# Kernel optimization log

Hardware: AMD Instinct MI355X
Metric: run time of the kernel (lower is better)

The kernel has to match this reference:

```python
import jax, jax.numpy as jnp
import numpy as np

PAD = -2.0 ** 16 + 1.0  # tf code uses -2**16+1 as masked logit
ITERATIONS = 3


def squash(x):
    # x: [..., out_units]
    n = jnp.sum(jnp.square(x), axis=-1, keepdims=True)
    return (n / (1.0 + n) / jnp.sqrt(n + 1e-9)) * x


def setup_inputs() -> dict:
    key = jax.random.key(0)
    k1, k2, k3, k4 = jax.random.split(key, 4)
    B, L, DIN, DOUT, K = 4096, 200, 64, 64, 8
    return {
        "low_capsule": jax.random.normal(k1, (B, L, DIN), dtype=jnp.float32),
        "seq_len": jax.random.randint(k2, (B, 1), 1, L + 1, dtype=jnp.int32),
        "B_matrix": jax.random.normal(k3, (1, K, L), dtype=jnp.float32),
        "S_matrix": jax.random.normal(k4, (DIN, DOUT), dtype=jnp.float32),
    }


def reference(low_capsule, seq_len, B_matrix, S_matrix):
    # low_capsule: [B, L, Din]; seq_len: [B, 1]; B_matrix: [1, K, L]; S_matrix: [Din, Dout]
    L = B_matrix.shape[2]
    # tf.sequence_mask(tile(seq_len,[1,K]), L) -> [B, K, L]; K axis broadcasts.
    mask = jnp.arange(L)[None, None, :] < seq_len[:, :, None]  # [B, 1, L]
    # low_capsule_new is identical every iteration; compute once.
    low_new = jnp.einsum('bli,io->blo', low_capsule, S_matrix)  # [B, L, Dout]
    Bc = B_matrix  # routing logits, updated (stateful assign_add in tf)
    high = None
    for _ in range(ITERATIONS):
        logits = jnp.where(mask, Bc, PAD)  # [B, K, L]
        W = jax.nn.softmax(logits, axis=-1)
        high = squash(jnp.einsum('bkl,blo->bko', W, low_new))  # [B, K, Dout]
        # B_delta = sum_b high @ low_new^T, keepdims on batch
        Bc = Bc + jnp.einsum('bko,blo->kl', high, low_new)[None]  # [1, K, L]
    return high
```

## Files before the change

### kernel.cpp

```cpp
#include <hip/hip_runtime.h>
#include <math.h>


#define B_SZ  4096
#define L_SZ  200
#define DK    64
#define K_SZ  8
#define KL    1600

__device__ __forceinline__ float rl(float x, int i) {
    return __int_as_float(__builtin_amdgcn_readlane(__float_as_int(x), i));
}

template<int INIT, int WRITE_BC>
__global__ __launch_bounds__(256) void k_table(const float* __restrict__ Bm,
                                               const float* __restrict__ S,
                                               const float* __restrict__ p2,
                                               const float* __restrict__ BcIn,
                                               float* __restrict__ BcOut,
                                               float* __restrict__ St,
                                               float* __restrict__ Wt) {
    int t = threadIdx.x;
    int blk = blockIdx.x;
    if (INIT && blk == 200) {
        for (int j = t; j < DK * DK; j += 256) {
            int o = j >> 6, ii = j & 63;
            St[j] = S[ii * DK + o];
        }
        return;
    }
    __shared__ float Bv[KL];
    __shared__ float mArr[K_SZ], rArr[K_SZ];
    int s = blk + 1;

    for (int j = t; j < KL; j += 256) {
        float bn;
        if (INIT) {
            bn = Bm[j];
        } else {
            float acc = 0.f;
            #pragma unroll
            for (int y = 0; y < 16; ++y) acc += p2[y * KL + j];
            bn = BcIn[j] + acc;
            if (WRITE_BC && blk == 0) BcOut[j] = bn;
        }
        Bv[j] = bn;
    }
    __syncthreads();

    int k = t >> 5, g = t & 31;
    const float* bk = &Bv[k * L_SZ];
    float m = -3.4e38f;
    for (int l = g; l < s; l += 32) m = fmaxf(m, bk[l]);
    #pragma unroll
    for (int st = 16; st; st >>= 1) m = fmaxf(m, __shfl_xor(m, st, 32));
    float sum = 0.f;
    for (int l = g; l < s; l += 32) sum += __expf(bk[l] - m);
    #pragma unroll
    for (int st = 16; st; st >>= 1) sum += __shfl_xor(sum, st, 32);
    if (g == 0) { mArr[k] = m; rArr[k] = 1.0f / sum; }
    __syncthreads();

    float* dst = Wt + (long)(s - 1) * KL;
    for (int j = t; j < KL; j += 256) {
        int l = j >> 3, kk = j & 7;
        dst[j] = (l < s) ? __expf(Bv[kk * L_SZ + l] - mArr[kk]) * rArr[kk] : 0.f;
    }
}

template<int WRITE_OUT>
__global__ __launch_bounds__(256, 6) void k_route6(const float* __restrict__ lc_g,
                                                   const int* __restrict__ seq_len,
                                                   const float* __restrict__ Wt_g,
                                                   const float* __restrict__ S_g,
                                                   const float* __restrict__ St_g,
                                                   float* __restrict__ partial,
                                                   float* __restrict__ out) {
    __shared__ float Wl[KL];
    __shared__ float hp_part[4][K_SZ][DK];
    __shared__ float hp_s[K_SZ][DK];
    __shared__ float hs_s[K_SZ][DK];
    int t = threadIdx.x;
    int b = blockIdx.x;
    const float* __restrict__ lcb = lc_g + (long)b * (L_SZ * DK);
    const float4* __restrict__ lc4 = (const float4*)lcb;
    int sl = seq_len[b];

    {
        const float4* __restrict__ src =
            (const float4*)(Wt_g + (long)(sl - 1) * KL);
        float4* dst = (float4*)Wl;
        for (int j = t; j < KL / 4; j += 256) dst[j] = src[j];
    }
    __syncthreads();

    int grp = t >> 4;
    int w = t >> 6;
    float4 a[8];
    #pragma unroll
    for (int p = 0; p < 8; ++p) a[p] = make_float4(0.f, 0.f, 0.f, 0.f);

    #pragma unroll 4
    for (int j = 0; j < 12; ++j) {
        float4 v = lc4[t + 256 * j];
        int r = grp + 16 * j;
        float4 wa = *(const float4*)&Wl[r * 8];
        float4 wb = *(const float4*)&Wl[r * 8 + 4];
        float wk[8] = {wa.x, wa.y, wa.z, wa.w, wb.x, wb.y, wb.z, wb.w};
        #pragma unroll
        for (int p = 0; p < 8; ++p) {
            a[p].x = fmaf(wk[p], v.x, a[p].x);
            a[p].y = fmaf(wk[p], v.y, a[p].y);
            a[p].z = fmaf(wk[p], v.z, a[p].z);
            a[p].w = fmaf(wk[p], v.w, a[p].w);
        }
    }
    if (t < 128) {
        float4 v = lc4[t + 3072];
        int r = grp + 192;
        float4 wa = *(const float4*)&Wl[r * 8];
        float4 wb = *(const float4*)&Wl[r * 8 + 4];
        float wk[8] = {wa.x, wa.y, wa.z, wa.w, wb.x, wb.y, wb.z, wb.w};
        #pragma unroll
        for (int p = 0; p < 8; ++p) {
            a[p].x = fmaf(wk[p], v.x, a[p].x);
            a[p].y = fmaf(wk[p], v.y, a[p].y);
            a[p].z = fmaf(wk[p], v.z, a[p].z);
            a[p].w = fmaf(wk[p], v.w, a[p].w);
        }
    }

    #pragma unroll
    for (int p = 0; p < 8; ++p) {
        a[p].x += __shfl_xor(a[p].x, 16, 64);
        a[p].y += __shfl_xor(a[p].y, 16, 64);
        a[p].z += __shfl_xor(a[p].z, 16, 64);
        a[p].w += __shfl_xor(a[p].w, 16, 64);
        a[p].x += __shfl_xor(a[p].x, 32, 64);
        a[p].y += __shfl_xor(a[p].y, 32, 64);
        a[p].z += __shfl_xor(a[p].z, 32, 64);
        a[p].w += __shfl_xor(a[p].w, 32, 64);
    }
    if ((t & 63) < 16) {
        int c0 = (t & 15) * 4;
        #pragma unroll
        for (int p = 0; p < 8; ++p)
            *(float4*)&hp_part[w][p][c0] = a[p];
    }
    __syncthreads();

    {
        int kk = t >> 5, ii = (t & 31) * 2;
        float2 r2 = make_float2(0.f, 0.f);
        #pragma unroll
        for (int ww = 0; ww < 4; ++ww) {
            float2 p = *(const float2*)&hp_part[ww][kk][ii];
            r2.x += p.x; r2.y += p.y;
        }
        *(float2*)&hp_s[kk][ii] = r2;
    }
    __syncthreads();

    int k = t >> 5, g = t & 31;
    int lam = t & 63;
    float h0 = 0.f, h1 = 0.f;
    {
        const float* sp = S_g + 2 * g;
        #pragma unroll 8
        for (int i = 0; i < DK; ++i) {
            float pv = hp_s[k][i];
            float2 sv = *(const float2*)(sp + i * DK);
            h0 = fmaf(pv, sv.x, h0); h1 = fmaf(pv, sv.y, h1);
        }
        float nn = h0 * h0 + h1 * h1;
        #pragma unroll
        for (int st = 16; st; st >>= 1) nn += __shfl_xor(nn, st, 32);
        float sc = nn / ((1.0f + nn) * sqrtf(nn + 1e-9f));
        h0 *= sc; h1 *= sc;
    }
    if (WRITE_OUT) {
        float2* ob2 = (float2*)(out + (long)b * (K_SZ * DK) + k * DK);
        ob2[g] = make_float2(h0, h1);
        return;
    }
    *(float2*)&hp_s[k][2 * g] = make_float2(h0, h1);

    {
        float s0 = 0.f, s1 = 0.f;
        const float* stp = St_g + 2 * g;
        #pragma unroll 8
        for (int o = 0; o < DK; ++o) {
            float hv = hp_s[k][o];
            float2 sv = *(const float2*)(stp + o * DK);
            s0 = fmaf(hv, sv.x, s0); s1 = fmaf(hv, sv.y, s1);
        }
        *(float2*)&hs_s[k][2 * g] = make_float2(s0, s1);
    }
    __syncthreads();

    float hsr[K_SZ];
    #pragma unroll
    for (int kk = 0; kk < K_SZ; ++kk) hsr[kk] = hs_s[kk][lam];
    if (t < L_SZ) {
        const float4* row4 = (const float4*)(lcb + (long)t * DK);
        float aa[K_SZ] = {};
        #pragma unroll
        for (int i4 = 0; i4 < 16; ++i4) {
            float4 v = row4[i4];
            #pragma unroll
            for (int kk = 0; kk < K_SZ; ++kk) {
                aa[kk] = fmaf(rl(hsr[kk], 4 * i4 + 0), v.x,
                         fmaf(rl(hsr[kk], 4 * i4 + 1), v.y,
                         fmaf(rl(hsr[kk], 4 * i4 + 2), v.z,
                         fmaf(rl(hsr[kk], 4 * i4 + 3), v.w, aa[kk]))));
            }
        }
        float* pb = partial + (long)b * KL;
        #pragma unroll
        for (int kk = 0; kk < K_SZ; ++kk)
            pb[kk * L_SZ + t] = aa[kk];
    }
}

__global__ __launch_bounds__(256) void k_reduceA(const float* __restrict__ partial,
                                                 float* __restrict__ partial2) {
    __shared__ float red[256];
    int x = blockIdx.x % 50;
    int y = blockIdx.x / 50;
    int t = threadIdx.x;
    int i = x * 32 + (t & 31);
    int sub = t >> 5;
    float s = 0.f;
    for (int p = y * 256 + sub; p < (y + 1) * 256; p += 8)
        s += partial[(long)p * KL + i];
    red[t] = s;
    __syncthreads();
    for (int step = 4; step >= 1; step >>= 1) {
        if (sub < step) red[t] += red[t + step * 32];
        __syncthreads();
    }
    if (sub == 0) partial2[y * KL + i] = red[t];
}

extern "C" void kernel_launch(void* const* d_in, const int* in_sizes, int n_in,
                              void* d_out, int out_size, void* d_ws, size_t ws_size,
                              hipStream_t stream) {
    const float* lc = (const float*)d_in[0];
    const int*   sl = (const int*)d_in[1];
    const float* Bm = (const float*)d_in[2];
    const float* S  = (const float*)d_in[3];
    float* out = (float*)d_out;
    float* ws  = (float*)d_ws;

    float* St      = ws;
    float* Wt      = St + 4096;
    float* Bc      = Wt + 200 * KL;
    float* partial = Bc + KL;
    float* p2      = out;

    k_table<1,0><<<201, 256, 0, stream>>>(Bm, S, p2, Bm, Bc, St, Wt);

    k_route6<0><<<B_SZ, 256, 0, stream>>>(lc, sl, Wt, S, St, partial, out);
    k_reduceA  <<<800, 256, 0, stream>>>(partial, p2);
    k_table<0,1><<<200, 256, 0, stream>>>(Bm, S, p2, Bm, Bc, St, Wt);

    k_route6<0><<<B_SZ, 256, 0, stream>>>(lc, sl, Wt, S, St, partial, out);
    k_reduceA  <<<800, 256, 0, stream>>>(partial, p2);
    k_table<0,0><<<200, 256, 0, stream>>>(Bm, S, p2, Bc, Bc, St, Wt);

    k_route6<1><<<B_SZ, 256, 0, stream>>>(lc, sl, Wt, S, St, partial, out);
}
```

Before: 301.2 us.

## Keep low-capsule tile in registers and reuse it for routing-delta pass

Each block now loads its 200x64 low-capsule tile into registers once (13 float4 per thread) and reuses them for both the weighted-sum phase and the B-delta dot products. Previously the second phase reread the tile from global memory row by row with readlane broadcasts. The delta phase now computes partial dot products per 16-lane group and reduces them through padded shared memory, at the cost of two block barriers per chunk. Register pressure rises, so the occupancy hint drops from 6 to 4 blocks per CU, and shared memory is aliased to fit the staging buffer.

```diff
diff --git a/kernel.cpp b/kernel.cpp
--- a/kernel.cpp
+++ b/kernel.cpp
@@ -7,10 +7,6 @@
 #define DK    64
 #define K_SZ  8
 #define KL    1600
-
-__device__ __forceinline__ float rl(float x, int i) {
-    return __int_as_float(__builtin_amdgcn_readlane(__float_as_int(x), i));
-}
 
 template<int INIT, int WRITE_BC>
 __global__ __launch_bounds__(256) void k_table(const float* __restrict__ Bm,
@@ -69,21 +65,23 @@
 }
 
 template<int WRITE_OUT>
-__global__ __launch_bounds__(256, 6) void k_route6(const float* __restrict__ lc_g,
+__global__ __launch_bounds__(256, 4) void k_route7(const float* __restrict__ lc_g,
                                                    const int* __restrict__ seq_len,
                                                    const float* __restrict__ Wt_g,
                                                    const float* __restrict__ S_g,
                                                    const float* __restrict__ St_g,
                                                    float* __restrict__ partial,
                                                    float* __restrict__ out) {
-    __shared__ float Wl[KL];
-    __shared__ float hp_part[4][K_SZ][DK];
+    __shared__ float smem[3648];
     __shared__ float hp_s[K_SZ][DK];
     __shared__ float hs_s[K_SZ][DK];
+    float* Wl = smem;
+    float* hp_part = smem + 1600;
+
     int t = threadIdx.x;
     int b = blockIdx.x;
-    const float* __restrict__ lcb = lc_g + (long)b * (L_SZ * DK);
-    const float4* __restrict__ lc4 = (const float4*)lcb;
+    const float4* __restrict__ lc4 =
+        (const float4*)(lc_g + (long)b * (L_SZ * DK));
     int sl = seq_len[b];
 
     {
@@ -96,37 +94,28 @@
 
     int grp = t >> 4;
     int w = t >> 6;
+
+    float4 v[13];
+    #pragma unroll
+    for (int j = 0; j < 12; ++j) v[j] = lc4[t + 256 * j];
+    if (t < 128) v[12] = lc4[t + 3072];
+    else         v[12] = make_float4(0.f, 0.f, 0.f, 0.f);
+
     float4 a[8];
     #pragma unroll
     for (int p = 0; p < 8; ++p) a[p] = make_float4(0.f, 0.f, 0.f, 0.f);
-
-    #pragma unroll 4
-    for (int j = 0; j < 12; ++j) {
-        float4 v = lc4[t + 256 * j];
-        int r = grp + 16 * j;
+    #pragma unroll
+    for (int j = 0; j < 13; ++j) {
+        int r = (j == 12) ? ((t < 128) ? 192 + grp : 199) : grp + 16 * j;
         float4 wa = *(const float4*)&Wl[r * 8];
         float4 wb = *(const float4*)&Wl[r * 8 + 4];
         float wk[8] = {wa.x, wa.y, wa.z, wa.w, wb.x, wb.y, wb.z, wb.w};
         #pragma unroll
         for (int p = 0; p < 8; ++p) {
-            a[p].x = fmaf(wk[p], v.x, a[p].x);
-            a[p].y = fmaf(wk[p], v.y, a[p].y);
-            a[p].z = fmaf(wk[p], v.z, a[p].z);
-            a[p].w = fmaf(wk[p], v.w, a[p].w);
-        }
-    }
-    if (t < 128) {
-        float4 v = lc4[t + 3072];
-        int r = grp + 192;
-        float4 wa = *(const float4*)&Wl[r * 8];
-        float4 wb = *(const float4*)&Wl[r * 8 + 4];
-        float wk[8] = {wa.x, wa.y, wa.z, wa.w, wb.x, wb.y, wb.z, wb.w};
-        #pragma unroll
-        for (int p = 0; p < 8; ++p) {
-            a[p].x = fmaf(wk[p], v.x, a[p].x);
-            a[p].y = fmaf(wk[p], v.y, a[p].y);
-            a[p].z = fmaf(wk[p], v.z, a[p].z);
-            a[p].w = fmaf(wk[p], v.w, a[p].w);
+            a[p].x = fmaf(wk[p], v[j].x, a[p].x);
+            a[p].y = fmaf(wk[p], v[j].y, a[p].y);
+            a[p].z = fmaf(wk[p], v[j].z, a[p].z);
+            a[p].w = fmaf(wk[p], v[j].w, a[p].w);
         }
     }
 
@@ -145,7 +134,7 @@
         int c0 = (t & 15) * 4;
         #pragma unroll
         for (int p = 0; p < 8; ++p)
-            *(float4*)&hp_part[w][p][c0] = a[p];
+            *(float4*)&hp_part[w * 512 + p * 64 + c0] = a[p];
     }
     __syncthreads();
 
@@ -154,7 +143,7 @@
         float2 r2 = make_float2(0.f, 0.f);
         #pragma unroll
         for (int ww = 0; ww < 4; ++ww) {
-            float2 p = *(const float2*)&hp_part[ww][kk][ii];
+            float2 p = *(const float2*)&hp_part[ww * 512 + kk * 64 + ii];
             r2.x += p.x; r2.y += p.y;
         }
         *(float2*)&hp_s[kk][ii] = r2;
@@ -162,7 +151,6 @@
     __syncthreads();
 
     int k = t >> 5, g = t & 31;
-    int lam = t & 63;
     float h0 = 0.f, h1 = 0.f;
     {
         const float* sp = S_g + 2 * g;
@@ -198,27 +186,39 @@
     }
     __syncthreads();
 
-    float hsr[K_SZ];
-    #pragma unroll
-    for (int kk = 0; kk < K_SZ; ++kk) hsr[kk] = hs_s[kk][lam];
-    if (t < L_SZ) {
-        const float4* row4 = (const float4*)(lcb + (long)t * DK);
-        float aa[K_SZ] = {};
-        #pragma unroll
-        for (int i4 = 0; i4 < 16; ++i4) {
-            float4 v = row4[i4];
+    float4 hs4[8];
+    int c0 = 4 * (t & 15);
+    #pragma unroll
+    for (int kk = 0; kk < 8; ++kk)
+        hs4[kk] = *(const float4*)&hs_s[kk][c0];
+
+    float* pb = partial + (long)b * KL;
+    int lane16 = t & 15;
+    #pragma unroll
+    for (int j = 0; j < 13; ++j) {
+        if (j < 12 || t < 128) {
             #pragma unroll
-            for (int kk = 0; kk < K_SZ; ++kk) {
-                aa[kk] = fmaf(rl(hsr[kk], 4 * i4 + 0), v.x,
-                         fmaf(rl(hsr[kk], 4 * i4 + 1), v.y,
-                         fmaf(rl(hsr[kk], 4 * i4 + 2), v.z,
-                         fmaf(rl(hsr[kk], 4 * i4 + 3), v.w, aa[kk]))));
+            for (int kk = 0; kk < 8; ++kk) {
+                float4 h = hs4[kk];
+                float p = v[j].x * h.x + v[j].y * h.y + v[j].z * h.z + v[j].w * h.w;
+                smem[(grp * 8 + kk) * 18 + lane16] = p;
             }
         }
-        float* pb = partial + (long)b * KL;
-        #pragma unroll
-        for (int kk = 0; kk < K_SZ; ++kk)
-            pb[kk * L_SZ + t] = aa[kk];
+        __syncthreads();
+        int nOut = (j < 12) ? 128 : 64;
+        if (t < nOut) {
+            int s = t >> 3, kk = t & 7;
+            int r = 16 * j + s;
+            const float2* q = (const float2*)&smem[(s * 8 + kk) * 18];
+            float2 q0 = q[0], q1 = q[1], q2 = q[2], q3 = q[3];
+            float2 q4 = q[4], q5 = q[5], q6 = q[6], q7 = q[7];
+            float sum = ((q0.x + q0.y) + (q1.x + q1.y))
+                      + ((q2.x + q2.y) + (q3.x + q3.y))
+                      + ((q4.x + q4.y) + (q5.x + q5.y))
+                      + ((q6.x + q6.y) + (q7.x + q7.y));
+            pb[kk * L_SZ + r] = sum;
+        }
+        __syncthreads();
     }
 }
 
@@ -260,13 +260,13 @@
 
     k_table<1,0><<<201, 256, 0, stream>>>(Bm, S, p2, Bm, Bc, St, Wt);
 
-    k_route6<0><<<B_SZ, 256, 0, stream>>>(lc, sl, Wt, S, St, partial, out);
+    k_route7<0><<<B_SZ, 256, 0, stream>>>(lc, sl, Wt, S, St, partial, out);
     k_reduceA  <<<800, 256, 0, stream>>>(partial, p2);
     k_table<0,1><<<200, 256, 0, stream>>>(Bm, S, p2, Bm, Bc, St, Wt);
 
-    k_route6<0><<<B_SZ, 256, 0, stream>>>(lc, sl, Wt, S, St, partial, out);
+    k_route7<0><<<B_SZ, 256, 0, stream>>>(lc, sl, Wt, S, St, partial, out);
     k_reduceA  <<<800, 256, 0, stream>>>(partial, p2);
     k_table<0,0><<<200, 256, 0, stream>>>(Bm, S, p2, Bc, Bc, St, Wt);
 
-    k_route6<1><<<B_SZ, 256, 0, stream>>>(lc, sl, Wt, S, St, partial, out);
-}
+    k_route7<1><<<B_SZ, 256, 0, stream>>>(lc, sl, Wt, S, St, partial, out);
+}
```

Result: faster. 278.7 us, median of 2 (-7.5%).
